# Kernel tuning notes

Hardware: AMD Instinct MI355X
Metric: run time of the kernel (lower is better)

Reference implementation:

```python
import jax, jax.numpy as jnp
import numpy as np

EPS = 1e-4  # CustomLayerNorm eps used by MaskedNorm


def setup_inputs() -> dict:
    key = jax.random.key(0)
    k1, k2, k3 = jax.random.split(key, 3)
    B, T, C = 8, 4096, 1024
    y = jax.random.normal(k1, (B, T, C), dtype=jnp.float32)
    mask = jax.random.randint(k2, (B, 1, T), 0, 2, dtype=jnp.int32)
    gamma = jax.random.uniform(k3, (C,), dtype=jnp.float32)
    beta = jnp.zeros((C,), dtype=jnp.float32)
    return {"y": y, "mask": mask, "gamma": gamma, "beta": beta}


def reference(y, mask, gamma, beta):
    # y: [B, T, C]; mask: [B, 1, T] (>0 means valid token)
    B, T, C = y.shape
    m = (mask.reshape(B, T) > 0)                      # [B, T] per-token mask
    mf = m.astype(y.dtype)[..., None]                 # [B, T, 1]
    n = jnp.sum(mf)                                   # number of selected tokens
    # Per-channel stats over selected tokens (torch .mean(0)/.std(0), ddof=1)
    mean = jnp.sum(y * mf, axis=(0, 1)) / n           # [C]
    diff = (y - mean) * mf                            # zero at masked-out rows
    var = jnp.sum(diff * diff, axis=(0, 1)) / (n - 1.0)
    std = jnp.sqrt(var)                               # [C]
    normed = gamma * ((y - mean) / (std + EPS)) + beta
    # masked_scatter: normalized values at valid rows, original y elsewhere
    return jnp.where(m[..., None], normed, y)
```

## Files before the change

kernel.cpp:

```cpp
#include <hip/hip_runtime.h>
#include <math.h>

#define MN_EPS 1e-4f

__device__ inline void f4add(float4& a, const float4& b) {
    a.x += b.x; a.y += b.y; a.z += b.z; a.w += b.w;
}

#define MN_CHUNK 256
__global__ void __launch_bounds__(256) mn_stats(
    const float4* __restrict__ y4, const int* __restrict__ mask,
    float4* __restrict__ pSum, float4* __restrict__ pSq,
    float* __restrict__ pCnt, int rowsPerBlock, int C4)
{
    __shared__ int sMask[MN_CHUNK];
    const int tid = threadIdx.x;
    const int b = blockIdx.x;
    const long r0 = (long)b * rowsPerBlock;
    float4 s = make_float4(0.f, 0.f, 0.f, 0.f);
    float4 q = make_float4(0.f, 0.f, 0.f, 0.f);
    int cnt = 0;
    for (int base = 0; base < rowsPerBlock; base += MN_CHUNK) {
        const int mrows = min(MN_CHUNK, rowsPerBlock - base);
        __syncthreads();
        for (int t = tid; t < mrows; t += blockDim.x)
            sMask[t] = mask[r0 + base + t];
        __syncthreads();
        for (int i = 0; i < mrows; ++i) {
            if (sMask[i] > 0) {
                ++cnt;
                const float4 v = y4[(r0 + base + i) * C4 + tid];
                s.x += v.x; s.y += v.y; s.z += v.z; s.w += v.w;
                q.x = fmaf(v.x, v.x, q.x);
                q.y = fmaf(v.y, v.y, q.y);
                q.z = fmaf(v.z, v.z, q.z);
                q.w = fmaf(v.w, v.w, q.w);
            }
        }
    }
    pSum[(long)b * C4 + tid] = s;
    pSq [(long)b * C4 + tid] = q;
    if (tid == 0) pCnt[b] = (float)cnt;
}

__global__ void __launch_bounds__(256) mn_finalize(
    const float4* __restrict__ pSum4, const float4* __restrict__ pSq4,
    const float* __restrict__ pCnt,
    const float4* __restrict__ gamma4, const float4* __restrict__ beta4,
    float4* __restrict__ aArr4, float4* __restrict__ bArr4, int P, int C4)
{
    __shared__ float4 sS[256];
    __shared__ float4 sQ[256];
    __shared__ float  sN[256];
    const int tid = threadIdx.x;
    const int c4 = blockIdx.x;

    float4 s = make_float4(0.f, 0.f, 0.f, 0.f);
    float4 q = make_float4(0.f, 0.f, 0.f, 0.f);
    float  n = 0.f;
    for (int p = tid; p < P; p += 256) {
        f4add(s, pSum4[(size_t)p * C4 + c4]);
        f4add(q, pSq4 [(size_t)p * C4 + c4]);
        n += pCnt[p];
    }
    sS[tid] = s; sQ[tid] = q; sN[tid] = n;
    __syncthreads();
    for (int off = 128; off > 0; off >>= 1) {
        if (tid < off) {
            f4add(sS[tid], sS[tid + off]);
            f4add(sQ[tid], sQ[tid + off]);
            sN[tid] += sN[tid + off];
        }
        __syncthreads();
    }
    if (tid == 0) {
        const float nn = sN[0];
        const float4 S = sS[0];
        const float4 Q = sQ[0];
        const float4 G = gamma4[c4];
        const float4 Bt = beta4[c4];
        float4 A, Bo;
        {
            const float mean = S.x / nn;
            float var = (Q.x - S.x * S.x / nn) / (nn - 1.0f);
            var = fmaxf(var, 0.0f);
            A.x = G.x / (sqrtf(var) + MN_EPS);
            Bo.x = Bt.x - mean * A.x;
        }
        {
            const float mean = S.y / nn;
            float var = (Q.y - S.y * S.y / nn) / (nn - 1.0f);
            var = fmaxf(var, 0.0f);
            A.y = G.y / (sqrtf(var) + MN_EPS);
            Bo.y = Bt.y - mean * A.y;
        }
        {
            const float mean = S.z / nn;
            float var = (Q.z - S.z * S.z / nn) / (nn - 1.0f);
            var = fmaxf(var, 0.0f);
            A.z = G.z / (sqrtf(var) + MN_EPS);
            Bo.z = Bt.z - mean * A.z;
        }
        {
            const float mean = S.w / nn;
            float var = (Q.w - S.w * S.w / nn) / (nn - 1.0f);
            var = fmaxf(var, 0.0f);
            A.w = G.w / (sqrtf(var) + MN_EPS);
            Bo.w = Bt.w - mean * A.w;
        }
        aArr4[c4] = A;
        bArr4[c4] = Bo;
    }
}

__global__ void __launch_bounds__(256) mn_apply(
    const float4* __restrict__ y4, const int* __restrict__ mask,
    const float4* __restrict__ aArr4, const float4* __restrict__ bArr4,
    float4* __restrict__ out4, int R, int C4)
{
    const int tid = threadIdx.x;
    const float4 A = aArr4[tid];
    const float4 Bv = bArr4[tid];
    for (int r = blockIdx.x; r < R; r += gridDim.x) {
        const float4 v = y4[(long)r * C4 + tid];
        float4 o;
        if (mask[r] > 0) {
            o.x = fmaf(A.x, v.x, Bv.x);
            o.y = fmaf(A.y, v.y, Bv.y);
            o.z = fmaf(A.z, v.z, Bv.z);
            o.w = fmaf(A.w, v.w, Bv.w);
        } else {
            o = v;
        }
        out4[(long)r * C4 + tid] = o;
    }
}

extern "C" void kernel_launch(void* const* d_in, const int* in_sizes, int n_in,
                              void* d_out, int out_size, void* d_ws, size_t ws_size,
                              hipStream_t stream)
{
    const float* y     = (const float*)d_in[0];
    const int*   mask  = (const int*)  d_in[1];
    const float* gamma = (const float*)d_in[2];
    const float* beta  = (const float*)d_in[3];
    float* out = (float*)d_out;

    const int R  = in_sizes[1];
    const int C  = in_sizes[2];
    const int C4 = C / 4;

    int P = 1024;
    while (P > 1) {
        const size_t need = ((size_t)2 * P * C + P + 2 * C) * sizeof(float);
        if (need <= ws_size && (R % P) == 0) break;
        P >>= 1;
    }
    const int rowsPerBlock = R / P;

    float* w    = (float*)d_ws;
    float* pSum = w;
    float* pSq  = pSum + (size_t)P * C;
    float* pCnt = pSq  + (size_t)P * C;
    float* aArr = pCnt + P;
    float* bArr = aArr + C;

    mn_stats<<<P, C4, 0, stream>>>((const float4*)y, mask,
                                   (float4*)pSum, (float4*)pSq, pCnt,
                                   rowsPerBlock, C4);

    mn_finalize<<<C4, 256, 0, stream>>>((const float4*)pSum, (const float4*)pSq,
                                        pCnt, (const float4*)gamma,
                                        (const float4*)beta,
                                        (float4*)aArr, (float4*)bArr, P, C4);

    mn_apply<<<2048, C4, 0, stream>>>((const float4*)y, mask,
                                      (const float4*)aArr, (const float4*)bArr,
                                      (float4*)out, R, C4);
}
```

Measured before the change: 264.3 us.

## Make stats loop branchless and use contiguous-row blocks with nontemporal stores in apply

Result: slower. 270.1 us (+2.2%).

```diff
diff --git a/kernel.cpp b/kernel.cpp
--- a/kernel.cpp
+++ b/kernel.cpp
@@ -2,6 +2,8 @@
 #include <math.h>
 
 #define MN_EPS 1e-4f
+
+typedef float v4f __attribute__((ext_vector_type(4)));
 
 __device__ inline void f4add(float4& a, const float4& b) {
     a.x += b.x; a.y += b.y; a.z += b.z; a.w += b.w;
@@ -13,34 +15,44 @@
     float4* __restrict__ pSum, float4* __restrict__ pSq,
     float* __restrict__ pCnt, int rowsPerBlock, int C4)
 {
-    __shared__ int sMask[MN_CHUNK];
+    __shared__ float sMaskF[MN_CHUNK];
+    __shared__ float sCnt[256];
     const int tid = threadIdx.x;
     const int b = blockIdx.x;
     const long r0 = (long)b * rowsPerBlock;
     float4 s = make_float4(0.f, 0.f, 0.f, 0.f);
     float4 q = make_float4(0.f, 0.f, 0.f, 0.f);
-    int cnt = 0;
+    float lc = 0.f;
     for (int base = 0; base < rowsPerBlock; base += MN_CHUNK) {
         const int mrows = min(MN_CHUNK, rowsPerBlock - base);
         __syncthreads();
-        for (int t = tid; t < mrows; t += blockDim.x)
-            sMask[t] = mask[r0 + base + t];
+        for (int t = tid; t < mrows; t += 256) {
+            const float mf = (mask[r0 + base + t] > 0) ? 1.0f : 0.0f;
+            sMaskF[t] = mf;
+            lc += mf;
+        }
         __syncthreads();
+        #pragma unroll 4
         for (int i = 0; i < mrows; ++i) {
-            if (sMask[i] > 0) {
-                ++cnt;
-                const float4 v = y4[(r0 + base + i) * C4 + tid];
-                s.x += v.x; s.y += v.y; s.z += v.z; s.w += v.w;
-                q.x = fmaf(v.x, v.x, q.x);
-                q.y = fmaf(v.y, v.y, q.y);
-                q.z = fmaf(v.z, v.z, q.z);
-                q.w = fmaf(v.w, v.w, q.w);
-            }
+            const float mf = sMaskF[i];
+            const float4 v = y4[(r0 + base + i) * C4 + tid];
+            const float4 mv = make_float4(mf * v.x, mf * v.y, mf * v.z, mf * v.w);
+            s.x += mv.x; s.y += mv.y; s.z += mv.z; s.w += mv.w;
+            q.x = fmaf(mv.x, v.x, q.x);
+            q.y = fmaf(mv.y, v.y, q.y);
+            q.z = fmaf(mv.z, v.z, q.z);
+            q.w = fmaf(mv.w, v.w, q.w);
         }
     }
     pSum[(long)b * C4 + tid] = s;
     pSq [(long)b * C4 + tid] = q;
-    if (tid == 0) pCnt[b] = (float)cnt;
+    sCnt[tid] = lc;
+    __syncthreads();
+    for (int off = 128; off > 0; off >>= 1) {
+        if (tid < off) sCnt[tid] += sCnt[tid + off];
+        __syncthreads();
+    }
+    if (tid == 0) pCnt[b] = sCnt[0];
 }
 
 __global__ void __launch_bounds__(256) mn_finalize(
@@ -82,29 +94,25 @@
         float4 A, Bo;
         {
             const float mean = S.x / nn;
-            float var = (Q.x - S.x * S.x / nn) / (nn - 1.0f);
-            var = fmaxf(var, 0.0f);
+            float var = fmaxf((Q.x - S.x * S.x / nn) / (nn - 1.0f), 0.0f);
             A.x = G.x / (sqrtf(var) + MN_EPS);
             Bo.x = Bt.x - mean * A.x;
         }
         {
             const float mean = S.y / nn;
-            float var = (Q.y - S.y * S.y / nn) / (nn - 1.0f);
-            var = fmaxf(var, 0.0f);
+            float var = fmaxf((Q.y - S.y * S.y / nn) / (nn - 1.0f), 0.0f);
             A.y = G.y / (sqrtf(var) + MN_EPS);
             Bo.y = Bt.y - mean * A.y;
         }
         {
             const float mean = S.z / nn;
-            float var = (Q.z - S.z * S.z / nn) / (nn - 1.0f);
-            var = fmaxf(var, 0.0f);
+            float var = fmaxf((Q.z - S.z * S.z / nn) / (nn - 1.0f), 0.0f);
             A.z = G.z / (sqrtf(var) + MN_EPS);
             Bo.z = Bt.z - mean * A.z;
         }
         {
             const float mean = S.w / nn;
-            float var = (Q.w - S.w * S.w / nn) / (nn - 1.0f);
-            var = fmaxf(var, 0.0f);
+            float var = fmaxf((Q.w - S.w * S.w / nn) / (nn - 1.0f), 0.0f);
             A.w = G.w / (sqrtf(var) + MN_EPS);
             Bo.w = Bt.w - mean * A.w;
         }
@@ -116,23 +124,23 @@
 __global__ void __launch_bounds__(256) mn_apply(
     const float4* __restrict__ y4, const int* __restrict__ mask,
     const float4* __restrict__ aArr4, const float4* __restrict__ bArr4,
-    float4* __restrict__ out4, int R, int C4)
+    float4* __restrict__ out4, int rowsPerBlock, int C4)
 {
     const int tid = threadIdx.x;
-    const float4 A = aArr4[tid];
+    const float4 A  = aArr4[tid];
     const float4 Bv = bArr4[tid];
-    for (int r = blockIdx.x; r < R; r += gridDim.x) {
-        const float4 v = y4[(long)r * C4 + tid];
-        float4 o;
-        if (mask[r] > 0) {
-            o.x = fmaf(A.x, v.x, Bv.x);
-            o.y = fmaf(A.y, v.y, Bv.y);
-            o.z = fmaf(A.z, v.z, Bv.z);
-            o.w = fmaf(A.w, v.w, Bv.w);
-        } else {
-            o = v;
-        }
-        out4[(long)r * C4 + tid] = o;
+    const long r0 = (long)blockIdx.x * rowsPerBlock;
+    #pragma unroll 2
+    for (int i = 0; i < rowsPerBlock; ++i) {
+        const long r = r0 + i;
+        const bool m = mask[r] > 0;
+        const float4 v = y4[r * C4 + tid];
+        v4f o;
+        o.x = m ? fmaf(A.x, v.x, Bv.x) : v.x;
+        o.y = m ? fmaf(A.y, v.y, Bv.y) : v.y;
+        o.z = m ? fmaf(A.z, v.z, Bv.z) : v.z;
+        o.w = m ? fmaf(A.w, v.w, Bv.w) : v.w;
+        __builtin_nontemporal_store(o, (v4f*)&out4[r * C4 + tid]);
     }
 }
 
@@ -174,7 +182,9 @@
                                         (const float4*)beta,
                                         (float4*)aArr, (float4*)bArr, P, C4);
 
-    mn_apply<<<2048, C4, 0, stream>>>((const float4*)y, mask,
-                                      (const float4*)aArr, (const float4*)bArr,
-                                      (float4*)out, R, C4);
+    int rpbA = 8;
+    while ((R % rpbA) != 0 && rpbA > 1) rpbA >>= 1;
+    mn_apply<<<R / rpbA, C4, 0, stream>>>((const float4*)y, mask,
+                                          (const float4*)aArr, (const float4*)bArr,
+                                          (float4*)out, rpbA, C4);
 }
```
